# Kernel tuning notes

Measured on AMD Instinct MI355X. Metric: run time of the kernel, lower is better.

Reference implementation:

```python
import jax, jax.numpy as jnp
import numpy as np

N, E, F_IN, HD, H, G, NG, OUT = 50000, 800000, 128, 64, 4, 512, 50, 64
HC = HD * H  # 256
LN_EPS = 1e-5

def _lin(k, fi, fo):
    return jax.random.normal(k, (fi, fo), jnp.float32) / np.sqrt(fi).astype(np.float32)

def setup_inputs() -> dict:
    key = jax.random.key(0)
    ks = jax.random.split(key, 26)
    x = jax.random.normal(ks[0], (N, F_IN), jnp.float32)
    edge_index = jax.random.randint(ks[1], (2, E), 0, N)
    batch = jnp.sort(jax.random.randint(ks[2], (N,), 0, G))
    group_ids = jax.random.randint(ks[3], (N,), 0, NG)
    inp = {
        'x': x, 'edge_index': edge_index, 'batch': batch, 'group_ids': group_ids,
        'group_table': jax.random.normal(ks[4], (NG, HD), jnp.float32),
        'inW': _lin(ks[5], F_IN + HD, HD), 'inb': jnp.zeros((HD,), jnp.float32),
        'inln_g': jnp.ones((HD,), jnp.float32), 'inln_b': jnp.zeros((HD,), jnp.float32),
        'W0': _lin(ks[6], HD, HC), 'as0': jax.random.normal(ks[7], (H, HD), jnp.float32) * 0.1,
        'ad0': jax.random.normal(ks[8], (H, HD), jnp.float32) * 0.1, 'b0': jnp.zeros((HC,), jnp.float32),
        'ln0g': jnp.ones((HC,), jnp.float32), 'ln0b': jnp.zeros((HC,), jnp.float32),
        'W1': _lin(ks[9], HC, HC), 'as1': jax.random.normal(ks[10], (H, HD), jnp.float32) * 0.1,
        'ad1': jax.random.normal(ks[11], (H, HD), jnp.float32) * 0.1, 'b1': jnp.zeros((HC,), jnp.float32),
        'ln1g': jnp.ones((HC,), jnp.float32), 'ln1b': jnp.zeros((HC,), jnp.float32),
        'fc1W': _lin(ks[12], HC, HD), 'fc1b': jnp.zeros((HD,), jnp.float32),
        'fc2W': _lin(ks[13], HD, OUT), 'fc2b': jnp.zeros((OUT,), jnp.float32),
    }
    return inp

def _layer_norm(x, g, b):
    mu = jnp.mean(x, axis=-1, keepdims=True)
    var = jnp.mean(jnp.square(x - mu), axis=-1, keepdims=True)
    return (x - mu) * jax.lax.rsqrt(var + LN_EPS) * g + b

def _gat_conv(x, src, dst, W, a_src, a_dst, bias):
    # x: [N, Fin] -> per-head projection [N, H, HD]
    xl = (x @ W).reshape(-1, H, HD)
    al_s = jnp.einsum('nhc,hc->nh', xl, a_src)  # [N, H]
    al_d = jnp.einsum('nhc,hc->nh', xl, a_dst)
    e = jax.nn.leaky_relu(al_s[src] + al_d[dst], 0.2)  # [Etot, H]
    m = jax.ops.segment_max(e, dst, num_segments=N)    # stable softmax over in-edges
    ex = jnp.exp(e - m[dst])
    s = jax.ops.segment_sum(ex, dst, num_segments=N)
    alpha = ex / (s[dst] + 1e-16)
    msg = xl[src] * alpha[:, :, None]                   # [Etot, H, HD]
    out = jax.ops.segment_sum(msg, dst, num_segments=N)
    return out.reshape(-1, HC) + bias

def reference(x, edge_index, batch, group_ids, group_table, inW, inb, inln_g, inln_b,
              W0, as0, ad0, b0, ln0g, ln0b, W1, as1, ad1, b1, ln1g, ln1b,
              fc1W, fc1b, fc2W, fc2b):
    # group embedding concat + input projection (Linear -> LN -> GELU)
    h = jnp.concatenate([x, group_table[group_ids]], axis=-1)
    h = jax.nn.gelu(_layer_norm(h @ inW + inb, inln_g, inln_b), approximate=False)
    # add self-loops (PyG GATConv default)
    loop = jnp.arange(N)
    src = jnp.concatenate([edge_index[0], loop])
    dst = jnp.concatenate([edge_index[1], loop])
    # layer 0: dims 64 -> 256, no residual (width mismatch)
    h = jax.nn.gelu(_layer_norm(_gat_conv(h, src, dst, W0, as0, ad0, b0), ln0g, ln0b), approximate=False)
    # layer 1: 256 -> 256, residual applies
    identity = h
    h = jax.nn.gelu(_layer_norm(_gat_conv(h, src, dst, W1, as1, ad1, b1), ln1g, ln1b), approximate=False)
    h = h + identity
    # global mean pool over graphs
    sums = jax.ops.segment_sum(h, batch, num_segments=G)
    cnt = jax.ops.segment_sum(jnp.ones((N, 1), h.dtype), batch, num_segments=G)
    pooled = sums / jnp.maximum(cnt, 1.0)
    z = jax.nn.gelu(pooled @ fc1W + fc1b, approximate=False)
    logits = z @ fc2W + fc2b
    return jax.nn.log_softmax(logits, axis=1)
```

## Files before the change

### kernel.cpp

```cpp
#include <hip/hip_runtime.h>
#include <math.h>

#define N_NODES 50000
#define N_EDGES 800000
#define ETOT (N_EDGES + N_NODES)
#define F_IN 128
#define HD 64
#define NHEAD 4
#define HC 256
#define NGRAPH 512
#define NOUT 64
#define LN_EPS 1e-5f

typedef __attribute__((ext_vector_type(8))) short bf16x8;
typedef __attribute__((ext_vector_type(4))) float f32x4;
typedef __attribute__((ext_vector_type(2))) float f32x2;

__device__ __forceinline__ float wave_sum(float v) {
#pragma unroll
    for (int m = 1; m < 64; m <<= 1) v += __shfl_xor(v, m, 64);
    return v;
}
__device__ __forceinline__ float wave_max(float v) {
#pragma unroll
    for (int m = 1; m < 64; m <<= 1) v = fmaxf(v, __shfl_xor(v, m, 64));
    return v;
}
__device__ __forceinline__ float red16(float v) {
    v += __shfl_xor(v, 1, 64);
    v += __shfl_xor(v, 2, 64);
    v += __shfl_xor(v, 4, 64);
    v += __shfl_xor(v, 8, 64);
    return v;
}
__device__ __forceinline__ float gelu_exact(float x) {
    return 0.5f * x * (1.0f + erff(x * 0.70710678118654752f));
}
__device__ __forceinline__ unsigned short f2bf(float x) {
    unsigned int u = __float_as_uint(x);
    return (unsigned short)((u + 0x7fffu + ((u >> 16) & 1u)) >> 16);
}
__device__ __forceinline__ float bf2f(unsigned short u) {
    return __uint_as_float(((unsigned int)u) << 16);
}

__global__ void k_count(const int* __restrict__ ei, int* __restrict__ deg) {
    int t = blockIdx.x * blockDim.x + threadIdx.x;
    if (t >= ETOT) return;
    int dst = (t < N_EDGES) ? ei[N_EDGES + t] : (t - N_EDGES);
    atomicAdd(deg + dst, 1);
}

__global__ void k_scan(const int* __restrict__ deg, int* __restrict__ rowptr,
                       int* __restrict__ cursor) {
    __shared__ int wsum[16];
    __shared__ int chunk_total;
    int tid = threadIdx.x, wid = tid >> 6, lane = tid & 63;
    int carry = 0;
    if (tid == 0) rowptr[0] = 0;
    for (int base = 0; base < N_NODES; base += 1024) {
        int i = base + tid;
        int v = (i < N_NODES) ? deg[i] : 0;
        int incl = v;
#pragma unroll
        for (int off = 1; off < 64; off <<= 1) {
            int t = __shfl_up(incl, off, 64);
            if (lane >= off) incl += t;
        }
        if (lane == 63) wsum[wid] = incl;
        __syncthreads();
        if (wid == 0) {
            int wv = (lane < 16) ? wsum[lane] : 0;
            int wincl = wv;
#pragma unroll
            for (int off = 1; off < 16; off <<= 1) {
                int t = __shfl_up(wincl, off, 64);
                if (lane >= off) wincl += t;
            }
            if (lane < 16) wsum[lane] = wincl - wv;
            if (lane == 15) chunk_total = wincl;
        }
        __syncthreads();
        int total_incl = carry + wsum[wid] + incl;
        if (i < N_NODES) {
            rowptr[i + 1] = total_incl;
            cursor[i] = total_incl - v;
        }
        carry += chunk_total;
        __syncthreads();
    }
}

__global__ void k_fill(const int* __restrict__ ei, int* __restrict__ cursor,
                       int* __restrict__ csr) {
    int t = blockIdx.x * blockDim.x + threadIdx.x;
    if (t >= ETOT) return;
    int src, dst;
    if (t < N_EDGES) { src = ei[t]; dst = ei[N_EDGES + t]; }
    else             { src = t - N_EDGES; dst = src; }
    int p = atomicAdd(cursor + dst, 1);
    csr[p] = src;
}

__global__ void k_prep(const float* __restrict__ x, const int* __restrict__ gid,
                       const float* __restrict__ gt, unsigned short* __restrict__ Ain) {
    int wid = threadIdx.x >> 6, lane = threadIdx.x & 63;
    int node = blockIdx.x * 4 + wid;
    float f0 = x[node * F_IN + lane];
    float f1 = x[node * F_IN + 64 + lane];
    int g = gid[node];
    float f2 = gt[g * HD + lane];
    unsigned short* r = Ain + (size_t)node * 192;
    r[lane] = f2bf(f0);
    r[64 + lane] = f2bf(f1);
    r[128 + lane] = f2bf(f2);
}

__global__ void k_pack_all(const float* __restrict__ inW, const float* __restrict__ W0,
                           const float* __restrict__ W1, const float* __restrict__ as0,
                           const float* __restrict__ ad0,
                           unsigned short* __restrict__ inWpk, unsigned short* __restrict__ W0pk,
                           unsigned short* __restrict__ W1pk, float* __restrict__ us,
                           float* __restrict__ ud) {
    int b = blockIdx.x;
    if (b < 48) {
        int tid = b * 256 + threadIdx.x;
        int i = tid & 7, l = (tid >> 3) & 63, t2 = tid >> 9;
        int nb = t2 % 4, kt = t2 / 4;
        int k = kt * 32 + ((l >> 4) << 3) + i;
        int n = nb * 16 + (l & 15);
        inWpk[tid] = f2bf(inW[k * 64 + n]);
    } else if (b < 112) {
        int tid = (b - 48) * 256 + threadIdx.x;
        int i = tid & 7, l = (tid >> 3) & 63, t2 = tid >> 9;
        int nb = t2 % 16, kt = t2 / 16;
        int q = kt * 32 + ((l >> 4) << 3) + i;
        int k = 16 * (q & 3) + (q >> 2);
        int n = nb * 16 + (l & 15);
        W0pk[tid] = f2bf(W0[k * 256 + n]);
    } else if (b < 368) {
        int tid = (b - 112) * 256 + threadIdx.x;
        int i = tid & 7, l = (tid >> 3) & 63, t2 = tid >> 9;
        int nb = t2 % 16, kt = t2 / 16;
        int k = kt * 32 + ((l >> 4) << 3) + i;
        int n = nb * 16 + (l & 15);
        W1pk[tid] = f2bf(W1[k * 256 + n]);
    } else {
        int t = threadIdx.x;
        int h = t >> 6, k2 = t & 63;
        float ss = 0.f, dd = 0.f;
        for (int c = 0; c < 64; c++) {
            float w = W0[k2 * 256 + h * 64 + c];
            ss += w * as0[h * 64 + c];
            dd += w * ad0[h * 64 + c];
        }
        us[t] = ss;
        ud[t] = dd;
    }
}

__global__ void k_proj_in_mma(const unsigned short* __restrict__ A,
                              const unsigned short* __restrict__ Wpk,
                              const float* __restrict__ inb, const float* __restrict__ lng,
                              const float* __restrict__ lnb, const float* __restrict__ us,
                              const float* __restrict__ ud, unsigned int* __restrict__ h08,
                              float* __restrict__ als0, float* __restrict__ ald0) {
    int wid = threadIdx.x >> 6, lane = threadIdx.x & 63;
    int m0 = blockIdx.x * 64 + wid * 16;
    if (m0 >= N_NODES) return;
    int g16 = lane >> 4, c16 = lane & 15;
    f32x4 acc[4] = {{0,0,0,0},{0,0,0,0},{0,0,0,0},{0,0,0,0}};
#pragma unroll
    for (int kt = 0; kt < 6; kt++) {
        bf16x8 a = *(const bf16x8*)(A + (size_t)(m0 + c16) * 192 + kt * 32 + g16 * 8);
#pragma unroll
        for (int nt = 0; nt < 4; nt++) {
            bf16x8 b = *(const bf16x8*)(Wpk + (((kt * 4 + nt) * 64 + lane) << 3));
            acc[nt] = __builtin_amdgcn_mfma_f32_16x16x32_bf16(a, b, acc[nt], 0, 0, 0);
        }
    }
    float bv[4], gv[4], bb[4];
    float usl[4][4], udl[4][4];
#pragma unroll
    for (int nt = 0; nt < 4; nt++) {
        int c = nt * 16 + c16;
        bv[nt] = inb[c]; gv[nt] = lng[c]; bb[nt] = lnb[c];
#pragma unroll
        for (int h = 0; h < 4; h++) {
            usl[h][nt] = us[h * 64 + c];
            udl[h][nt] = ud[h * 64 + c];
        }
    }
#pragma unroll
    for (int j = 0; j < 4; j++) {
        float d[4], s = 0.f;
#pragma unroll
        for (int nt = 0; nt < 4; nt++) { d[nt] = acc[nt][j] + bv[nt]; s += d[nt]; }
        float mu = red16(s) * (1.0f / 64.0f);
        float v = 0.f;
#pragma unroll
        for (int nt = 0; nt < 4; nt++) { d[nt] -= mu; v += d[nt] * d[nt]; }
        float r = rsqrtf(red16(v) * (1.0f / 64.0f) + LN_EPS);
        int row = m0 + g16 * 4 + j;
        float y0 = gelu_exact(d[0] * r * gv[0] + bb[0]);
        float y1 = gelu_exact(d[1] * r * gv[1] + bb[1]);
        float y2 = gelu_exact(d[2] * r * gv[2] + bb[2]);
        float y3 = gelu_exact(d[3] * r * gv[3] + bb[3]);
        int u = __builtin_amdgcn_cvt_pk_fp8_f32(y0, y1, 0, false);
        u = __builtin_amdgcn_cvt_pk_fp8_f32(y2, y3, u, true);
        h08[(size_t)row * 16 + c16] = (unsigned int)u;
        float ps0 = y0 * usl[0][0] + y1 * usl[0][1] + y2 * usl[0][2] + y3 * usl[0][3];
        float ps1 = y0 * usl[1][0] + y1 * usl[1][1] + y2 * usl[1][2] + y3 * usl[1][3];
        float ps2 = y0 * usl[2][0] + y1 * usl[2][1] + y2 * usl[2][2] + y3 * usl[2][3];
        float ps3 = y0 * usl[3][0] + y1 * usl[3][1] + y2 * usl[3][2] + y3 * usl[3][3];
        float pd0 = y0 * udl[0][0] + y1 * udl[0][1] + y2 * udl[0][2] + y3 * udl[0][3];
        float pd1 = y0 * udl[1][0] + y1 * udl[1][1] + y2 * udl[1][2] + y3 * udl[1][3];
        float pd2 = y0 * udl[2][0] + y1 * udl[2][1] + y2 * udl[2][2] + y3 * udl[2][3];
        float pd3 = y0 * udl[3][0] + y1 * udl[3][1] + y2 * udl[3][2] + y3 * udl[3][3];
        ps0 = red16(ps0); ps1 = red16(ps1); ps2 = red16(ps2); ps3 = red16(ps3);
        pd0 = red16(pd0); pd1 = red16(pd1); pd2 = red16(pd2); pd3 = red16(pd3);
        if (c16 == 0) {
            float4 s4 = {ps0, ps1, ps2, ps3};
            float4 d4 = {pd0, pd1, pd2, pd3};
            ((float4*)als0)[row] = s4;
            ((float4*)ald0)[row] = d4;
        }
    }
}

__global__ void k_agg0(const int* __restrict__ rowptr, const int* __restrict__ csr,
                       const unsigned int* __restrict__ h08, const float* __restrict__ als,
                       const float* __restrict__ ald, unsigned short* __restrict__ aggbf) {
    __shared__ float4 lacc[2][64];
    __shared__ float lss[2][4];
    int wid = threadIdx.x >> 6, lane = threadIdx.x & 63;
    int nloc = wid >> 1, half = wid & 1;
    int node = blockIdx.x * 2 + nloc;
    int start = rowptr[node], end = rowptr[node + 1];
    int g = lane >> 4, l16 = lane & 15;
    float4 adv = ((const float4*)ald)[node];
    int cntE = end - start;
    int mid = start + ((cntE + 1) >> 1);
    int k0 = half ? mid : start;
    int k1 = half ? end : mid;
    float a00 = 0, a01 = 0, a02 = 0, a03 = 0;
    float a10 = 0, a11 = 0, a12 = 0, a13 = 0;
    float a20 = 0, a21 = 0, a22 = 0, a23 = 0;
    float a30 = 0, a31 = 0, a32 = 0, a33 = 0;
    float s0 = 0, s1 = 0, s2 = 0, s3 = 0;
    const float4* als4 = (const float4*)als;
    for (int kb = k0; kb < k1; kb += 8) {
        int eA = kb + g, eB = kb + 4 + g;
        int cA = (eA < k1) ? eA : (k1 - 1);
        int cB = (eB < k1) ? eB : (k1 - 1);
        int snA = csr[cA], snB = csr[cB];
        float4 avA = als4[snA], avB = als4[snB];
        unsigned int uA = h08[(size_t)snA * 16 + l16];
        unsigned int uB = h08[(size_t)snB * 16 + l16];
        float eA0 = avA.x + adv.x; eA0 = fmaxf(eA0, 0.2f * eA0);
        float eA1 = avA.y + adv.y; eA1 = fmaxf(eA1, 0.2f * eA1);
        float eA2 = avA.z + adv.z; eA2 = fmaxf(eA2, 0.2f * eA2);
        float eA3 = avA.w + adv.w; eA3 = fmaxf(eA3, 0.2f * eA3);
        float wA0 = __expf(eA0), wA1 = __expf(eA1), wA2 = __expf(eA2), wA3 = __expf(eA3);
        if (eA >= k1) { wA0 = 0.f; wA1 = 0.f; wA2 = 0.f; wA3 = 0.f; }
        f32x2 loA = __builtin_amdgcn_cvt_pk_f32_fp8((int)uA, false);
        f32x2 hiA = __builtin_amdgcn_cvt_pk_f32_fp8((int)uA, true);
        s0 += wA0; s1 += wA1; s2 += wA2; s3 += wA3;
        float x0 = loA.x, x1 = loA.y, x2 = hiA.x, x3 = hiA.y;
        a00 += wA0 * x0; a01 += wA0 * x1; a02 += wA0 * x2; a03 += wA0 * x3;
        a10 += wA1 * x0; a11 += wA1 * x1; a12 += wA1 * x2; a13 += wA1 * x3;
        a20 += wA2 * x0; a21 += wA2 * x1; a22 += wA2 * x2; a23 += wA2 * x3;
        a30 += wA3 * x0; a31 += wA3 * x1; a32 += wA3 * x2; a33 += wA3 * x3;
        float eB0 = avB.x + adv.x; eB0 = fmaxf(eB0, 0.2f * eB0);
        float eB1 = avB.y + adv.y; eB1 = fmaxf(eB1, 0.2f * eB1);
        float eB2 = avB.z + adv.z; eB2 = fmaxf(eB2, 0.2f * eB2);
        float eB3 = avB.w + adv.w; eB3 = fmaxf(eB3, 0.2f * eB3);
        float wB0 = __expf(eB0), wB1 = __expf(eB1), wB2 = __expf(eB2), wB3 = __expf(eB3);
        if (eB >= k1) { wB0 = 0.f; wB1 = 0.f; wB2 = 0.f; wB3 = 0.f; }
        f32x2 loB = __builtin_amdgcn_cvt_pk_f32_fp8((int)uB, false);
        f32x2 hiB = __builtin_amdgcn_cvt_pk_f32_fp8((int)uB, true);
        s0 += wB0; s1 += wB1; s2 += wB2; s3 += wB3;
        float z0 = loB.x, z1 = loB.y, z2 = hiB.x, z3 = hiB.y;
        a00 += wB0 * z0; a01 += wB0 * z1; a02 += wB0 * z2; a03 += wB0 * z3;
        a10 += wB1 * z0; a11 += wB1 * z1; a12 += wB1 * z2; a13 += wB1 * z3;
        a20 += wB2 * z0; a21 += wB2 * z1; a22 += wB2 * z2; a23 += wB2 * z3;
        a30 += wB3 * z0; a31 += wB3 * z1; a32 += wB3 * z2; a33 += wB3 * z3;
    }
#define RED2(v) v += __shfl_xor(v, 16, 64); v += __shfl_xor(v, 32, 64)
    RED2(a00); RED2(a01); RED2(a02); RED2(a03);
    RED2(a10); RED2(a11); RED2(a12); RED2(a13);
    RED2(a20); RED2(a21); RED2(a22); RED2(a23);
    RED2(a30); RED2(a31); RED2(a32); RED2(a33);
    RED2(s0);  RED2(s1);  RED2(s2);  RED2(s3);
#undef RED2
    if (half) {
        float o0 = (g == 0) ? a00 : (g == 1) ? a10 : (g == 2) ? a20 : a30;
        float o1 = (g == 0) ? a01 : (g == 1) ? a11 : (g == 2) ? a21 : a31;
        float o2 = (g == 0) ? a02 : (g == 1) ? a12 : (g == 2) ? a22 : a32;
        float o3 = (g == 0) ? a03 : (g == 1) ? a13 : (g == 2) ? a23 : a33;
        float4 o = {o0, o1, o2, o3};
        lacc[nloc][lane] = o;
        if (lane < 4) {
            float sv = (lane == 0) ? s0 : (lane == 1) ? s1 : (lane == 2) ? s2 : s3;
            lss[nloc][lane] = sv;
        }
    }
    __syncthreads();
    if (!half) {
        float4 p0 = lacc[nloc][0 + l16];
        float4 p1 = lacc[nloc][16 + l16];
        float4 p2 = lacc[nloc][32 + l16];
        float4 p3 = lacc[nloc][48 + l16];
        a00 += p0.x; a01 += p0.y; a02 += p0.z; a03 += p0.w;
        a10 += p1.x; a11 += p1.y; a12 += p1.z; a13 += p1.w;
        a20 += p2.x; a21 += p2.y; a22 += p2.z; a23 += p2.w;
        a30 += p3.x; a31 += p3.y; a32 += p3.z; a33 += p3.w;
        s0 += lss[nloc][0]; s1 += lss[nloc][1];
        s2 += lss[nloc][2]; s3 += lss[nloc][3];
        float o0 = (g == 0) ? a00 : (g == 1) ? a10 : (g == 2) ? a20 : a30;
        float o1 = (g == 0) ? a01 : (g == 1) ? a11 : (g == 2) ? a21 : a31;
        float o2 = (g == 0) ? a02 : (g == 1) ? a12 : (g == 2) ? a22 : a32;
        float o3 = (g == 0) ? a03 : (g == 1) ? a13 : (g == 2) ? a23 : a33;
        float sg = (g == 0) ? s0 : (g == 1) ? s1 : (g == 2) ? s2 : s3;
        float inv = 1.0f / (sg + 1e-16f);
        ushort4 o = {f2bf(o0 * inv), f2bf(o1 * inv), f2bf(o2 * inv), f2bf(o3 * inv)};
        ((ushort4*)aggbf)[(size_t)node * 64 + lane] = o;
    }
}

__global__ void k_postgemm0(const unsigned short* __restrict__ A,
                            const unsigned short* __restrict__ Wpk,
                            const float* __restrict__ bias, const float* __restrict__ lng,
                            const float* __restrict__ lnb, unsigned short* __restrict__ h1bf) {
    int wid = threadIdx.x >> 6, lane = threadIdx.x & 63;
    int m0 = blockIdx.x * 64 + wid * 16;
    if (m0 >= N_NODES) return;
    int g16 = lane >> 4, c16 = lane & 15;
    f32x4 acc[16] = {};
#pragma unroll
    for (int h = 0; h < 4; h++) {
#pragma unroll
        for (int kt = 0; kt < 2; kt++) {
            bf16x8 a = *(const bf16x8*)(A + (size_t)(m0 + c16) * 256 + h * 64 + kt * 32 + g16 * 8);
#pragma unroll
            for (int nt = 0; nt < 4; nt++) {
                bf16x8 b = *(const bf16x8*)(Wpk + (((kt * 16 + h * 4 + nt) * 64 + lane) << 3));
                acc[h * 4 + nt] = __builtin_amdgcn_mfma_f32_16x16x32_bf16(a, b, acc[h * 4 + nt], 0, 0, 0);
            }
        }
    }
    float bv[16], gv[16], bb[16];
#pragma unroll
    for (int q = 0; q < 16; q++) {
        int c = q * 16 + c16;
        bv[q] = bias[c]; gv[q] = lng[c]; bb[q] = lnb[c];
    }
#pragma unroll
    for (int j = 0; j < 4; j++) {
        float d[16], ssum = 0.f;
#pragma unroll
        for (int q = 0; q < 16; q++) { d[q] = acc[q][j] + bv[q]; ssum += d[q]; }
        float mu = red16(ssum) * (1.0f / 256.0f);
        float v = 0.f;
#pragma unroll
        for (int q = 0; q < 16; q++) { d[q] -= mu; v += d[q] * d[q]; }
        float r = rsqrtf(red16(v) * (1.0f / 256.0f) + LN_EPS);
        int row = m0 + g16 * 4 + j;
#pragma unroll
        for (int q = 0; q < 16; q++) {
            float y = gelu_exact(d[q] * r * gv[q] + bb[q]);
            h1bf[(size_t)row * 256 + q * 16 + c16] = f2bf(y);
        }
    }
}

__global__ void k_proj_mma(const unsigned short* __restrict__ A,
                           const unsigned short* __restrict__ Wpk,
                           const float* __restrict__ as_, const float* __restrict__ ad_,
                           unsigned int* __restrict__ xl8, float* __restrict__ als,
                           float* __restrict__ ald) {
    int wid = threadIdx.x >> 6, lane = threadIdx.x & 63;
    int m0 = blockIdx.x * 16;
    int g16 = lane >> 4, c16 = lane & 15;
    f32x4 acc[4] = {{0,0,0,0},{0,0,0,0},{0,0,0,0},{0,0,0,0}};
#pragma unroll
    for (int kt = 0; kt < 8; kt++) {
        bf16x8 a = *(const bf16x8*)(A + (size_t)(m0 + c16) * 256 + kt * 32 + g16 * 8);
#pragma unroll
        for (int nt = 0; nt < 4; nt++) {
            bf16x8 b = *(const bf16x8*)(Wpk + (((kt * 16 + wid * 4 + nt) * 64 + lane) << 3));
            acc[nt] = __builtin_amdgcn_mfma_f32_16x16x32_bf16(a, b, acc[nt], 0, 0, 0);
        }
    }
    float asv[4], adv[4];
#pragma unroll
    for (int nt = 0; nt < 4; nt++) {
        int c = wid * 64 + nt * 16 + c16;
        asv[nt] = as_[c]; adv[nt] = ad_[c];
    }
#pragma unroll
    for (int j = 0; j < 4; j++) {
        int row = m0 + g16 * 4 + j;
        float v0 = acc[0][j], v1 = acc[1][j], v2 = acc[2][j], v3 = acc[3][j];
        int u = __builtin_amdgcn_cvt_pk_fp8_f32(v0, v1, 0, false);
        u = __builtin_amdgcn_cvt_pk_fp8_f32(v2, v3, u, true);
        xl8[(size_t)row * 64 + wid * 16 + c16] = (unsigned int)u;
        float ps = v0 * asv[0] + v1 * asv[1] + v2 * asv[2] + v3 * asv[3];
        float pd = v0 * adv[0] + v1 * adv[1] + v2 * adv[2] + v3 * adv[3];
        ps = red16(ps); pd = red16(pd);
        if (c16 == 0) { als[row * 4 + wid] = ps; ald[row * 4 + wid] = pd; }
    }
}

__global__ void k_agg1(const int* __restrict__ rowptr, const int* __restrict__ csr,
                       const unsigned int* __restrict__ xl8, const float* __restrict__ als,
                       const float* __restrict__ ald, const float* __restrict__ bias,
                       const float* __restrict__ lng, const float* __restrict__ lnb,
                       const unsigned short* __restrict__ identity_bf,
                       const int* __restrict__ batch, float* __restrict__ pooled,
                       int* __restrict__ cnt) {
    __shared__ float4 lacc[2][64];
    __shared__ float lss[2][64];
    __shared__ float4 lyout[2][64];
    __shared__ int lbatch[2];
    int wid = threadIdx.x >> 6, lane = threadIdx.x & 63;
    int nloc = wid >> 1, half = wid & 1;
    int node = blockIdx.x * 2 + nloc;
    int start = rowptr[node], end = rowptr[node + 1];
    int head = lane >> 4, c16 = lane & 15;
    int fb = head * 64 + c16;
    float adh = ald[node * 4 + head];
    int cntE = end - start;
    int mid = start + ((cntE + 1) >> 1);
    int k0 = half ? mid : start;
    int k1 = half ? end : mid;
    float4 acc = {0.f, 0.f, 0.f, 0.f};
    float s = 0.f;
    int k = k0;
    for (; k + 8 <= k1; k += 8) {
        int sn0 = csr[k],     sn1 = csr[k + 1], sn2 = csr[k + 2], sn3 = csr[k + 3];
        int sn4 = csr[k + 4], sn5 = csr[k + 5], sn6 = csr[k + 6], sn7 = csr[k + 7];
        float e0 = als[sn0 * 4 + head], e1 = als[sn1 * 4 + head];
        float e2 = als[sn2 * 4 + head], e3 = als[sn3 * 4 + head];
        float e4 = als[sn4 * 4 + head], e5 = als[sn5 * 4 + head];
        float e6 = als[sn6 * 4 + head], e7 = als[sn7 * 4 + head];
        unsigned int u0 = xl8[(size_t)sn0 * 64 + lane], u1 = xl8[(size_t)sn1 * 64 + lane];
        unsigned int u2 = xl8[(size_t)sn2 * 64 + lane], u3 = xl8[(size_t)sn3 * 64 + lane];
        unsigned int u4 = xl8[(size_t)sn4 * 64 + lane], u5 = xl8[(size_t)sn5 * 64 + lane];
        unsigned int u6 = xl8[(size_t)sn6 * 64 + lane], u7 = xl8[(size_t)sn7 * 64 + lane];
        e0 += adh; e1 += adh; e2 += adh; e3 += adh;
        e0 = fmaxf(e0, 0.2f * e0); e1 = fmaxf(e1, 0.2f * e1);
        e2 = fmaxf(e2, 0.2f * e2); e3 = fmaxf(e3, 0.2f * e3);
        float a0 = __expf(e0), a1 = __expf(e1), a2 = __expf(e2), a3 = __expf(e3);
        s += a0 + a1 + a2 + a3;
        f32x2 lo0 = __builtin_amdgcn_cvt_pk_f32_fp8((int)u0, false);
        f32x2 hi0 = __builtin_amdgcn_cvt_pk_f32_fp8((int)u0, true);
        f32x2 lo1 = __builtin_amdgcn_cvt_pk_f32_fp8((int)u1, false);
        f32x2 hi1 = __builtin_amdgcn_cvt_pk_f32_fp8((int)u1, true);
        f32x2 lo2 = __builtin_amdgcn_cvt_pk_f32_fp8((int)u2, false);
        f32x2 hi2 = __builtin_amdgcn_cvt_pk_f32_fp8((int)u2, true);
        f32x2 lo3 = __builtin_amdgcn_cvt_pk_f32_fp8((int)u3, false);
        f32x2 hi3 = __builtin_amdgcn_cvt_pk_f32_fp8((int)u3, true);
        acc.x += a0 * lo0.x + a1 * lo1.x + a2 * lo2.x + a3 * lo3.x;
        acc.y += a0 * lo0.y + a1 * lo1.y + a2 * lo2.y + a3 * lo3.y;
        acc.z += a0 * hi0.x + a1 * hi1.x + a2 * hi2.x + a3 * hi3.x;
        acc.w += a0 * hi0.y + a1 * hi1.y + a2 * hi2.y + a3 * hi3.y;
        e4 += adh; e5 += adh; e6 += adh; e7 += adh;
        e4 = fmaxf(e4, 0.2f * e4); e5 = fmaxf(e5, 0.2f * e5);
        e6 = fmaxf(e6, 0.2f * e6); e7 = fmaxf(e7, 0.2f * e7);
        float a4 = __expf(e4), a5 = __expf(e5), a6 = __expf(e6), a7 = __expf(e7);
        s += a4 + a5 + a6 + a7;
        f32x2 lo4 = __builtin_amdgcn_cvt_pk_f32_fp8((int)u4, false);
        f32x2 hi4 = __builtin_amdgcn_cvt_pk_f32_fp8((int)u4, true);
        f32x2 lo5 = __builtin_amdgcn_cvt_pk_f32_fp8((int)u5, false);
        f32x2 hi5 = __builtin_amdgcn_cvt_pk_f32_fp8((int)u5, true);
        f32x2 lo6 = __builtin_amdgcn_cvt_pk_f32_fp8((int)u6, false);
        f32x2 hi6 = __builtin_amdgcn_cvt_pk_f32_fp8((int)u6, true);
        f32x2 lo7 = __builtin_amdgcn_cvt_pk_f32_fp8((int)u7, false);
        f32x2 hi7 = __builtin_amdgcn_cvt_pk_f32_fp8((int)u7, true);
        acc.x += a4 * lo4.x + a5 * lo5.x + a6 * lo6.x + a7 * lo7.x;
        acc.y += a4 * lo4.y + a5 * lo5.y + a6 * lo6.y + a7 * lo7.y;
        acc.z += a4 * hi4.x + a5 * hi5.x + a6 * hi6.x + a7 * hi7.x;
        acc.w += a4 * hi4.y + a5 * hi5.y + a6 * hi6.y + a7 * hi7.y;
    }
    for (; k + 4 <= k1; k += 4) {
        int sn0 = csr[k], sn1 = csr[k + 1], sn2 = csr[k + 2], sn3 = csr[k + 3];
        float e0 = als[sn0 * 4 + head] + adh;
        float e1 = als[sn1 * 4 + head] + adh;
        float e2 = als[sn2 * 4 + head] + adh;
        float e3 = als[sn3 * 4 + head] + adh;
        unsigned int u0 = xl8[(size_t)sn0 * 64 + lane];
        unsigned int u1 = xl8[(size_t)sn1 * 64 + lane];
        unsigned int u2 = xl8[(size_t)sn2 * 64 + lane];
        unsigned int u3 = xl8[(size_t)sn3 * 64 + lane];
        e0 = fmaxf(e0, 0.2f * e0); e1 = fmaxf(e1, 0.2f * e1);
        e2 = fmaxf(e2, 0.2f * e2); e3 = fmaxf(e3, 0.2f * e3);
        float a0 = __expf(e0), a1 = __expf(e1), a2 = __expf(e2), a3 = __expf(e3);
        s += a0 + a1 + a2 + a3;
        f32x2 lo0 = __builtin_amdgcn_cvt_pk_f32_fp8((int)u0, false);
        f32x2 hi0 = __builtin_amdgcn_cvt_pk_f32_fp8((int)u0, true);
        f32x2 lo1 = __builtin_amdgcn_cvt_pk_f32_fp8((int)u1, false);
        f32x2 hi1 = __builtin_amdgcn_cvt_pk_f32_fp8((int)u1, true);
        f32x2 lo2 = __builtin_amdgcn_cvt_pk_f32_fp8((int)u2, false);
        f32x2 hi2 = __builtin_amdgcn_cvt_pk_f32_fp8((int)u2, true);
        f32x2 lo3 = __builtin_amdgcn_cvt_pk_f32_fp8((int)u3, false);
        f32x2 hi3 = __builtin_amdgcn_cvt_pk_f32_fp8((int)u3, true);
        acc.x += a0 * lo0.x + a1 * lo1.x + a2 * lo2.x + a3 * lo3.x;
        acc.y += a0 * lo0.y + a1 * lo1.y + a2 * lo2.y + a3 * lo3.y;
        acc.z += a0 * hi0.x + a1 * hi1.x + a2 * hi2.x + a3 * hi3.x;
        acc.w += a0 * hi0.y + a1 * hi1.y + a2 * hi2.y + a3 * hi3.y;
    }
    for (; k < k1; k++) {
        int sn = csr[k];
        float e = als[sn * 4 + head] + adh;
        e = fmaxf(e, 0.2f * e);
        float a = __expf(e);
        s += a;
        unsigned int u = xl8[(size_t)sn * 64 + lane];
        f32x2 lo = __builtin_amdgcn_cvt_pk_f32_fp8((int)u, false);
        f32x2 hi = __builtin_amdgcn_cvt_pk_f32_fp8((int)u, true);
        acc.x += a * lo.x; acc.y += a * lo.y;
        acc.z += a * hi.x; acc.w += a * hi.y;
    }
    if (half) { lacc[nloc][lane] = acc; lss[nloc][lane] = s; }
    __syncthreads();
    if (!half) {
        float4 p = lacc[nloc][lane];
        acc.x += p.x; acc.y += p.y; acc.z += p.z; acc.w += p.w;
        s += lss[nloc][lane];
        float inv = 1.0f / (s + 1e-16f);
        acc.x = acc.x * inv + bias[fb];
        acc.y = acc.y * inv + bias[fb + 16];
        acc.z = acc.z * inv + bias[fb + 32];
        acc.w = acc.w * inv + bias[fb + 48];
        float mu = wave_sum(acc.x + acc.y + acc.z + acc.w) * (1.0f / 256.0f);
        float dx = acc.x - mu, dy = acc.y - mu, dz = acc.z - mu, dw = acc.w - mu;
        float var = wave_sum(dx * dx + dy * dy + dz * dz + dw * dw) * (1.0f / 256.0f);
        float r = rsqrtf(var + LN_EPS);
        float g0v = lng[fb], g1v = lng[fb + 16], g2v = lng[fb + 32], g3v = lng[fb + 48];
        float b0v = lnb[fb], b1v = lnb[fb + 16], b2v = lnb[fb + 32], b3v = lnb[fb + 48];
        const unsigned short* idp = identity_bf + (size_t)node * 256 + fb;
        float4 y;
        y.x = gelu_exact(dx * r * g0v + b0v) + bf2f(idp[0]);
        y.y = gelu_exact(dy * r * g1v + b1v) + bf2f(idp[16]);
        y.z = gelu_exact(dz * r * g2v + b2v) + bf2f(idp[32]);
        y.w = gelu_exact(dw * r * g3v + b3v) + bf2f(idp[48]);
        lyout[nloc][lane] = y;
        if (lane == 0) lbatch[nloc] = batch[node];
    }
    __syncthreads();
    if (wid == 0) {
        int g0 = lbatch[0], g1 = lbatch[1];
        float4 a = lyout[0][lane], b = lyout[1][lane];
        float* p0 = pooled + (size_t)g0 * 256 + fb;
        if (g0 == g1) {
            atomicAdd(p0 +  0, a.x + b.x); atomicAdd(p0 + 16, a.y + b.y);
            atomicAdd(p0 + 32, a.z + b.z); atomicAdd(p0 + 48, a.w + b.w);
            if (lane == 0) atomicAdd(cnt + g0, 2);
        } else {
            float* p1 = pooled + (size_t)g1 * 256 + fb;
            atomicAdd(p0 +  0, a.x); atomicAdd(p0 + 16, a.y);
            atomicAdd(p0 + 32, a.z); atomicAdd(p0 + 48, a.w);
            atomicAdd(p1 +  0, b.x); atomicAdd(p1 + 16, b.y);
            atomicAdd(p1 + 32, b.z); atomicAdd(p1 + 48, b.w);
            if (lane == 0) { atomicAdd(cnt + g0, 1); atomicAdd(cnt + g1, 1); }
        }
    }
}

__global__ void k_final(const float* __restrict__ pooled, const int* __restrict__ cnt,
                        const float* __restrict__ fc1W, const float* __restrict__ fc1b,
                        const float* __restrict__ fc2W, const float* __restrict__ fc2b,
                        float* __restrict__ out) {
    __shared__ float prow[4][256];
    __shared__ float zrow[4][64];
    int wid = threadIdx.x >> 6, lane = threadIdx.x & 63;
    int g = blockIdx.x * 4 + wid;
    float inv = 1.0f / fmaxf((float)cnt[g], 1.0f);
#pragma unroll
    for (int k = lane; k < 256; k += 64) prow[wid][k] = pooled[g * 256 + k] * inv;
    __syncthreads();
    float acc = fc1b[lane];
#pragma unroll 4
    for (int k = 0; k < 256; k++) acc += prow[wid][k] * fc1W[k * 64 + lane];
    zrow[wid][lane] = gelu_exact(acc);
    __syncthreads();
    float logit = fc2b[lane];
#pragma unroll 4
    for (int k = 0; k < 64; k++) logit += zrow[wid][k] * fc2W[k * 64 + lane];
    float mx = wave_max(logit);
    float se = wave_sum(__expf(logit - mx));
    out[g * NOUT + lane] = logit - mx - logf(se);
}

extern "C" void kernel_launch(void* const* d_in, const int* in_sizes, int n_in,
                              void* d_out, int out_size, void* d_ws, size_t ws_size,
                              hipStream_t stream) {
    const float* x     = (const float*)d_in[0];
    const int*   ei    = (const int*)d_in[1];
    const int*   batch = (const int*)d_in[2];
    const int*   gid   = (const int*)d_in[3];
    const float* gt    = (const float*)d_in[4];
    const float* inW   = (const float*)d_in[5];
    const float* inb   = (const float*)d_in[6];
    const float* inlng = (const float*)d_in[7];
    const float* inlnb = (const float*)d_in[8];
    const float* W0    = (const float*)d_in[9];
    const float* as0   = (const float*)d_in[10];
    const float* ad0   = (const float*)d_in[11];
    const float* b0    = (const float*)d_in[12];
    const float* ln0g  = (const float*)d_in[13];
    const float* ln0b  = (const float*)d_in[14];
    const float* W1    = (const float*)d_in[15];
    const float* as1   = (const float*)d_in[16];
    const float* ad1   = (const float*)d_in[17];
    const float* b1    = (const float*)d_in[18];
    const float* ln1g  = (const float*)d_in[19];
    const float* ln1b  = (const float*)d_in[20];
    const float* fc1W  = (const float*)d_in[21];
    const float* fc1b  = (const float*)d_in[22];
    const float* fc2W  = (const float*)d_in[23];
    const float* fc2b  = (const float*)d_in[24];
    float* out = (float*)d_out;

    char* ws = (char*)d_ws;
    size_t off = 0;
    auto alloc = [&](size_t bytes) {
        void* p = ws + off;
        off += (bytes + 255) / 256 * 256;
        return p;
    };
    unsigned short* Ain    = (unsigned short*)alloc((size_t)N_NODES * 192 * 2);
    unsigned int*   h08    = (unsigned int*)alloc((size_t)N_NODES * 16 * 4);
    unsigned short* agg0bf = (unsigned short*)alloc((size_t)N_NODES * 256 * 2);
    unsigned short* h1bf   = (unsigned short*)alloc((size_t)N_NODES * 256 * 2);
    unsigned int*   xl8    = (unsigned int*)alloc((size_t)N_NODES * 64 * 4);
    unsigned short* inWpk  = (unsigned short*)alloc((size_t)192 * 64 * 2);
    unsigned short* W0pk   = (unsigned short*)alloc((size_t)64 * 256 * 2);
    unsigned short* W1pk   = (unsigned short*)alloc((size_t)256 * 256 * 2);
    float* us     = (float*)alloc((size_t)256 * 4);
    float* ud     = (float*)alloc((size_t)256 * 4);
    float* als0   = (float*)alloc((size_t)N_NODES * 4 * 4);
    float* ald0   = (float*)alloc((size_t)N_NODES * 4 * 4);
    float* als1   = (float*)alloc((size_t)N_NODES * 4 * 4);
    float* ald1   = (float*)alloc((size_t)N_NODES * 4 * 4);
    int*   rowptr = (int*)alloc((size_t)(N_NODES + 1) * 4);
    int*   cursor = (int*)alloc((size_t)N_NODES * 4);
    int*   csr    = (int*)alloc((size_t)ETOT * 4);
    float* pooled = (float*)alloc((size_t)NGRAPH * 256 * 4);
    int*   cnt    = (int*)alloc((size_t)NGRAPH * 4);
    int*   deg    = (int*)alloc((size_t)N_NODES * 4);
    size_t zspan = ((char*)deg + (size_t)N_NODES * 4) - (char*)pooled;

    hipMemsetAsync(pooled, 0, zspan, stream);

    int eb = (ETOT + 255) / 256;
    k_count<<<eb, 256, 0, stream>>>(ei, deg);
    k_scan<<<1, 1024, 0, stream>>>(deg, rowptr, cursor);
    k_fill<<<eb, 256, 0, stream>>>(ei, cursor, csr);

    k_prep<<<N_NODES / 4, 256, 0, stream>>>(x, gid, gt, Ain);
    k_pack_all<<<369, 256, 0, stream>>>(inW, W0, W1, as0, ad0, inWpk, W0pk, W1pk, us, ud);

    k_proj_in_mma<<<(N_NODES + 63) / 64, 256, 0, stream>>>(Ain, inWpk, inb, inlng, inlnb,
                                                           us, ud, h08, als0, ald0);
    k_agg0<<<N_NODES / 2, 256, 0, stream>>>(rowptr, csr, h08, als0, ald0, agg0bf);
    k_postgemm0<<<(N_NODES + 63) / 64, 256, 0, stream>>>(agg0bf, W0pk, b0, ln0g, ln0b, h1bf);
    k_proj_mma<<<N_NODES / 16, 256, 0, stream>>>(h1bf, W1pk, as1, ad1, xl8, als1, ald1);
    k_agg1<<<N_NODES / 2, 256, 0, stream>>>(rowptr, csr, xl8, als1, ald1, b1, ln1g, ln1b,
                                            h1bf, batch, pooled, cnt);
    k_final<<<NGRAPH / 4, 256, 0, stream>>>(pooled, cnt, fc1W, fc1b, fc2W, fc2b, out);
}
```

Before: 420.3 us.

## Fuse input prep into projection GEMM and split agg1 edges across four waves

Removes the separate prep kernel by loading x and group-table rows as fp32 inside the input projection MMA kernel and converting them to bf16 in registers, which drops the Ain write and re-read. The layer-1 aggregation now uses 512-thread blocks, so each node's in-edge range is split across four waves instead of two, and the partial sums are combined through shared memory. The 8-edge unrolled loop in that kernel is dropped, which lowers per-wave memory-level parallelism. The extra waves and the larger reduction add synchronisation and shared-memory overhead.

```diff
diff --git a/kernel.cpp b/kernel.cpp
--- a/kernel.cpp
+++ b/kernel.cpp
@@ -100,20 +100,6 @@
     else             { src = t - N_EDGES; dst = src; }
     int p = atomicAdd(cursor + dst, 1);
     csr[p] = src;
-}
-
-__global__ void k_prep(const float* __restrict__ x, const int* __restrict__ gid,
-                       const float* __restrict__ gt, unsigned short* __restrict__ Ain) {
-    int wid = threadIdx.x >> 6, lane = threadIdx.x & 63;
-    int node = blockIdx.x * 4 + wid;
-    float f0 = x[node * F_IN + lane];
-    float f1 = x[node * F_IN + 64 + lane];
-    int g = gid[node];
-    float f2 = gt[g * HD + lane];
-    unsigned short* r = Ain + (size_t)node * 192;
-    r[lane] = f2bf(f0);
-    r[64 + lane] = f2bf(f1);
-    r[128 + lane] = f2bf(f2);
 }
 
 __global__ void k_pack_all(const float* __restrict__ inW, const float* __restrict__ W0,
@@ -159,7 +145,8 @@
     }
 }
 
-__global__ void k_proj_in_mma(const unsigned short* __restrict__ A,
+__global__ void k_proj_in_mma(const float* __restrict__ x, const int* __restrict__ gid,
+                              const float* __restrict__ gt,
                               const unsigned short* __restrict__ Wpk,
                               const float* __restrict__ inb, const float* __restrict__ lng,
                               const float* __restrict__ lnb, const float* __restrict__ us,
@@ -169,10 +156,20 @@
     int m0 = blockIdx.x * 64 + wid * 16;
     if (m0 >= N_NODES) return;
     int g16 = lane >> 4, c16 = lane & 15;
+    int row_a = m0 + c16;
+    int g = gid[row_a];
     f32x4 acc[4] = {{0,0,0,0},{0,0,0,0},{0,0,0,0},{0,0,0,0}};
 #pragma unroll
     for (int kt = 0; kt < 6; kt++) {
-        bf16x8 a = *(const bf16x8*)(A + (size_t)(m0 + c16) * 192 + kt * 32 + g16 * 8);
+        const float* src = (kt < 4) ? (x + (size_t)row_a * F_IN + kt * 32 + g16 * 8)
+                                    : (gt + (size_t)g * HD + (kt - 4) * 32 + g16 * 8);
+        float4 f0 = *(const float4*)(src);
+        float4 f1 = *(const float4*)(src + 4);
+        bf16x8 a;
+        a[0] = (short)f2bf(f0.x); a[1] = (short)f2bf(f0.y);
+        a[2] = (short)f2bf(f0.z); a[3] = (short)f2bf(f0.w);
+        a[4] = (short)f2bf(f1.x); a[5] = (short)f2bf(f1.y);
+        a[6] = (short)f2bf(f1.z); a[7] = (short)f2bf(f1.w);
 #pragma unroll
         for (int nt = 0; nt < 4; nt++) {
             bf16x8 b = *(const bf16x8*)(Wpk + (((kt * 4 + nt) * 64 + lane) << 3));
@@ -419,70 +416,23 @@
                        const unsigned short* __restrict__ identity_bf,
                        const int* __restrict__ batch, float* __restrict__ pooled,
                        int* __restrict__ cnt) {
-    __shared__ float4 lacc[2][64];
-    __shared__ float lss[2][64];
+    __shared__ float4 lacc[2][3][64];
+    __shared__ float lss[2][3][64];
     __shared__ float4 lyout[2][64];
     __shared__ int lbatch[2];
     int wid = threadIdx.x >> 6, lane = threadIdx.x & 63;
-    int nloc = wid >> 1, half = wid & 1;
+    int nloc = wid >> 2, q = wid & 3;
     int node = blockIdx.x * 2 + nloc;
     int start = rowptr[node], end = rowptr[node + 1];
+    int len = end - start;
     int head = lane >> 4, c16 = lane & 15;
     int fb = head * 64 + c16;
     float adh = ald[node * 4 + head];
-    int cntE = end - start;
-    int mid = start + ((cntE + 1) >> 1);
-    int k0 = half ? mid : start;
-    int k1 = half ? end : mid;
+    int k0 = start + (len * q) / 4;
+    int k1 = start + (len * (q + 1)) / 4;
     float4 acc = {0.f, 0.f, 0.f, 0.f};
     float s = 0.f;
     int k = k0;
-    for (; k + 8 <= k1; k += 8) {
-        int sn0 = csr[k],     sn1 = csr[k + 1], sn2 = csr[k + 2], sn3 = csr[k + 3];
-        int sn4 = csr[k + 4], sn5 = csr[k + 5], sn6 = csr[k + 6], sn7 = csr[k + 7];
-        float e0 = als[sn0 * 4 + head], e1 = als[sn1 * 4 + head];
-        float e2 = als[sn2 * 4 + head], e3 = als[sn3 * 4 + head];
-        float e4 = als[sn4 * 4 + head], e5 = als[sn5 * 4 + head];
-        float e6 = als[sn6 * 4 + head], e7 = als[sn7 * 4 + head];
-        unsigned int u0 = xl8[(size_t)sn0 * 64 + lane], u1 = xl8[(size_t)sn1 * 64 + lane];
-        unsigned int u2 = xl8[(size_t)sn2 * 64 + lane], u3 = xl8[(size_t)sn3 * 64 + lane];
-        unsigned int u4 = xl8[(size_t)sn4 * 64 + lane], u5 = xl8[(size_t)sn5 * 64 + lane];
-        unsigned int u6 = xl8[(size_t)sn6 * 64 + lane], u7 = xl8[(size_t)sn7 * 64 + lane];
-        e0 += adh; e1 += adh; e2 += adh; e3 += adh;
-        e0 = fmaxf(e0, 0.2f * e0); e1 = fmaxf(e1, 0.2f * e1);
-        e2 = fmaxf(e2, 0.2f * e2); e3 = fmaxf(e3, 0.2f * e3);
-        float a0 = __expf(e0), a1 = __expf(e1), a2 = __expf(e2), a3 = __expf(e3);
-        s += a0 + a1 + a2 + a3;
-        f32x2 lo0 = __builtin_amdgcn_cvt_pk_f32_fp8((int)u0, false);
-        f32x2 hi0 = __builtin_amdgcn_cvt_pk_f32_fp8((int)u0, true);
-        f32x2 lo1 = __builtin_amdgcn_cvt_pk_f32_fp8((int)u1, false);
-        f32x2 hi1 = __builtin_amdgcn_cvt_pk_f32_fp8((int)u1, true);
-        f32x2 lo2 = __builtin_amdgcn_cvt_pk_f32_fp8((int)u2, false);
-        f32x2 hi2 = __builtin_amdgcn_cvt_pk_f32_fp8((int)u2, true);
-        f32x2 lo3 = __builtin_amdgcn_cvt_pk_f32_fp8((int)u3, false);
-        f32x2 hi3 = __builtin_amdgcn_cvt_pk_f32_fp8((int)u3, true);
-        acc.x += a0 * lo0.x + a1 * lo1.x + a2 * lo2.x + a3 * lo3.x;
-        acc.y += a0 * lo0.y + a1 * lo1.y + a2 * lo2.y + a3 * lo3.y;
-        acc.z += a0 * hi0.x + a1 * hi1.x + a2 * hi2.x + a3 * hi3.x;
-        acc.w += a0 * hi0.y + a1 * hi1.y + a2 * hi2.y + a3 * hi3.y;
-        e4 += adh; e5 += adh; e6 += adh; e7 += adh;
-        e4 = fmaxf(e4, 0.2f * e4); e5 = fmaxf(e5, 0.2f * e5);
-        e6 = fmaxf(e6, 0.2f * e6); e7 = fmaxf(e7, 0.2f * e7);
-        float a4 = __expf(e4), a5 = __expf(e5), a6 = __expf(e6), a7 = __expf(e7);
-        s += a4 + a5 + a6 + a7;
-        f32x2 lo4 = __builtin_amdgcn_cvt_pk_f32_fp8((int)u4, false);
-        f32x2 hi4 = __builtin_amdgcn_cvt_pk_f32_fp8((int)u4, true);
-        f32x2 lo5 = __builtin_amdgcn_cvt_pk_f32_fp8((int)u5, false);
-        f32x2 hi5 = __builtin_amdgcn_cvt_pk_f32_fp8((int)u5, true);
-        f32x2 lo6 = __builtin_amdgcn_cvt_pk_f32_fp8((int)u6, false);
-        f32x2 hi6 = __builtin_amdgcn_cvt_pk_f32_fp8((int)u6, true);
-        f32x2 lo7 = __builtin_amdgcn_cvt_pk_f32_fp8((int)u7, false);
-        f32x2 hi7 = __builtin_amdgcn_cvt_pk_f32_fp8((int)u7, true);
-        acc.x += a4 * lo4.x + a5 * lo5.x + a6 * lo6.x + a7 * lo7.x;
-        acc.y += a4 * lo4.y + a5 * lo5.y + a6 * lo6.y + a7 * lo7.y;
-        acc.z += a4 * hi4.x + a5 * hi5.x + a6 * hi6.x + a7 * hi7.x;
-        acc.w += a4 * hi4.y + a5 * hi5.y + a6 * hi6.y + a7 * hi7.y;
-    }
     for (; k + 4 <= k1; k += 4) {
         int sn0 = csr[k], sn1 = csr[k + 1], sn2 = csr[k + 2], sn3 = csr[k + 3];
         float e0 = als[sn0 * 4 + head] + adh;
@@ -522,12 +472,17 @@
         acc.x += a * lo.x; acc.y += a * lo.y;
         acc.z += a * hi.x; acc.w += a * hi.y;
     }
-    if (half) { lacc[nloc][lane] = acc; lss[nloc][lane] = s; }
+    if (q) { lacc[nloc][q - 1][lane] = acc; lss[nloc][q - 1][lane] = s; }
     __syncthreads();
-    if (!half) {
-        float4 p = lacc[nloc][lane];
-        acc.x += p.x; acc.y += p.y; acc.z += p.z; acc.w += p.w;
-        s += lss[nloc][lane];
+    if (q == 0) {
+        float4 p0 = lacc[nloc][0][lane];
+        float4 p1 = lacc[nloc][1][lane];
+        float4 p2 = lacc[nloc][2][lane];
+        acc.x += p0.x + p1.x + p2.x;
+        acc.y += p0.y + p1.y + p2.y;
+        acc.z += p0.z + p1.z + p2.z;
+        acc.w += p0.w + p1.w + p2.w;
+        s += lss[nloc][0][lane] + lss[nloc][1][lane] + lss[nloc][2][lane];
         float inv = 1.0f / (s + 1e-16f);
         acc.x = acc.x * inv + bias[fb];
         acc.y = acc.y * inv + bias[fb + 16];
@@ -630,7 +585,6 @@
         off += (bytes + 255) / 256 * 256;
         return p;
     };
-    unsigned short* Ain    = (unsigned short*)alloc((size_t)N_NODES * 192 * 2);
     unsigned int*   h08    = (unsigned int*)alloc((size_t)N_NODES * 16 * 4);
     unsigned short* agg0bf = (unsigned short*)alloc((size_t)N_NODES * 256 * 2);
     unsigned short* h1bf   = (unsigned short*)alloc((size_t)N_NODES * 256 * 2);
@@ -659,15 +613,14 @@
     k_scan<<<1, 1024, 0, stream>>>(deg, rowptr, cursor);
     k_fill<<<eb, 256, 0, stream>>>(ei, cursor, csr);
 
-    k_prep<<<N_NODES / 4, 256, 0, stream>>>(x, gid, gt, Ain);
     k_pack_all<<<369, 256, 0, stream>>>(inW, W0, W1, as0, ad0, inWpk, W0pk, W1pk, us, ud);
 
-    k_proj_in_mma<<<(N_NODES + 63) / 64, 256, 0, stream>>>(Ain, inWpk, inb, inlng, inlnb,
+    k_proj_in_mma<<<(N_NODES + 63) / 64, 256, 0, stream>>>(x, gid, gt, inWpk, inb, inlng, inlnb,
                                                            us, ud, h08, als0, ald0);
     k_agg0<<<N_NODES / 2, 256, 0, stream>>>(rowptr, csr, h08, als0, ald0, agg0bf);
     k_postgemm0<<<(N_NODES + 63) / 64, 256, 0, stream>>>(agg0bf, W0pk, b0, ln0g, ln0b, h1bf);
     k_proj_mma<<<N_NODES / 16, 256, 0, stream>>>(h1bf, W1pk, as1, ad1, xl8, als1, ald1);
-    k_agg1<<<N_NODES / 2, 256, 0, stream>>>(rowptr, csr, xl8, als1, ald1, b1, ln1g, ln1b,
+    k_agg1<<<N_NODES / 2, 512, 0, stream>>>(rowptr, csr, xl8, als1, ald1, b1, ln1g, ln1b,
                                             h1bf, batch, pooled, cnt);
     k_final<<<NGRAPH / 4, 256, 0, stream>>>(pooled, cnt, fc1W, fc1b, fc2W, fc2b, out);
 }
```

Measured after the change: 435.6 us. +3.6%, slower.
